# Kernel tuning notes

Measured on AMD Instinct MI355X. Metric: run time of the kernel, lower is better.

The kernel has to match this reference:

```python
import jax, jax.numpy as jnp
import numpy as np

B, S, D = 16, 1024, 64
BASE, SCALE = 10000.0, 1.0


def setup_inputs() -> dict:
    key = jax.random.key(0)
    # geospatial coordinates in [0, 1)
    spa_feat = jax.random.uniform(key, (B, S, 2), dtype=jnp.float32)
    return {"spa_feat": spa_feat}


def reference(spa_feat):
    d = D
    q = d // 4  # number of frequency bands per coordinate axis
    inv_freq = 1.0 / (BASE ** (jnp.arange(q, dtype=jnp.float32) / q))  # [q]
    xy = spa_feat * SCALE                                # [B,S,2]
    freq = xy[..., :, None] * inv_freq                   # [B,S,2,q]
    freq_x, freq_y = freq[..., 0, :], freq[..., 1, :]    # [B,S,q] each
    sin_emb = jnp.concatenate([jnp.sin(freq_x), jnp.sin(freq_y)], axis=-1)  # [B,S,d/2]
    cos_emb = jnp.concatenate([jnp.cos(freq_x), jnp.cos(freq_y)], axis=-1)  # [B,S,d/2]
    b, s, h = sin_emb.shape  # h = d//2 number of 2x2 blocks
    r = 2 * jnp.arange(h)    # top-left row/col index of each 2x2 block
    # Block-diagonal rotation matrix: block i = [[cos_i, -sin_i], [sin_i, cos_i]]
    R = jnp.zeros((b, s, d, d), dtype=sin_emb.dtype)
    R = (R.at[:, :, r, r].set(cos_emb)
           .at[:, :, r, r + 1].set(-sin_emb)
           .at[:, :, r + 1, r].set(sin_emb)
           .at[:, :, r + 1, r + 1].set(cos_emb))
    return R
```

## Files before the change

### kernel.cpp

```cpp
#include <hip/hip_runtime.h>


#define NBS 16384
#define MPB 8
#define NBLK (NBS / MPB)

typedef float vfloat4 __attribute__((ext_vector_type(4)));

__global__ __launch_bounds__(256) void rope2d_kernel(
    const float* __restrict__ spa,
    float* __restrict__ out)
{
    const int t   = threadIdx.x;
    const int bs0 = blockIdx.x * MPB;

    __shared__ float ssin[MPB * 32];
    __shared__ float scos[MPB * 32];

    {
        const int m = t >> 5;
        const int h = t & 31;
        const float xy   = spa[(bs0 + m) * 2 + (h >> 4)];
        const int   i    = h & 15;
        const float invf = exp2f(-(float)i * 0.83048202372184059f);
        float s, c;
        sincosf(xy * invf, &s, &c);
        ssin[t] = s;
        scos[t] = c;
    }
    __syncthreads();

    vfloat4* outv = (vfloat4*)out + (size_t)bs0 * 1024;
    const int cg = t & 15;

    #pragma unroll
    for (int k = 0; k < 32; ++k) {
        const int g   = t + k * 256;
        const int row = (g >> 4) & 63;
        vfloat4 v = (vfloat4)(0.f, 0.f, 0.f, 0.f);
        if ((row >> 2) == cg) {
            const int m = g >> 10;
            const int h = row >> 1;
            const float s = ssin[m * 32 + h];
            const float c = scos[m * 32 + h];
            const float e0 = (row & 1) ? s : c;
            const float e1 = (row & 1) ? c : -s;
            if (row & 2) { v.z = e0; v.w = e1; }
            else         { v.x = e0; v.y = e1; }
        }
        __builtin_nontemporal_store(v, &outv[g]);
    }
}

extern "C" void kernel_launch(void* const* d_in, const int* in_sizes, int n_in,
                              void* d_out, int out_size, void* d_ws, size_t ws_size,
                              hipStream_t stream) {
    const float* spa = (const float*)d_in[0];
    float* out = (float*)d_out;
    rope2d_kernel<<<NBLK, 256, 0, stream>>>(spa, out);
}
```

Baseline: 265.0 us.

## Zero output with memset and scatter only diagonal-block vectors

Fills the whole output with hipMemsetAsync, then launches a kernel that writes only the four float4 chunks per row around the 2x2 diagonal block instead of all sixteen. The aim is to move most of the zero-filling into the driver's fill path and cut the work each thread does. In exchange, the output is written twice (a full memset plus a partial scatter), which adds total memory traffic. It also adds a second launch and drops the nontemporal store hint.

```diff
diff --git a/kernel.cpp b/kernel.cpp
--- a/kernel.cpp
+++ b/kernel.cpp
@@ -7,7 +7,7 @@
 
 typedef float vfloat4 __attribute__((ext_vector_type(4)));
 
-__global__ __launch_bounds__(256) void rope2d_kernel(
+__global__ __launch_bounds__(256) void rope2d_scatter_kernel(
     const float* __restrict__ spa,
     float* __restrict__ out)
 {
@@ -31,24 +31,23 @@
     __syncthreads();
 
     vfloat4* outv = (vfloat4*)out + (size_t)bs0 * 1024;
-    const int cg = t & 15;
 
     #pragma unroll
-    for (int k = 0; k < 32; ++k) {
-        const int g   = t + k * 256;
-        const int row = (g >> 4) & 63;
+    for (int j = 0; j < MPB; ++j) {
+        const int idx = t + j * 256;
+        const int m   = idx >> 8;
+        const int r   = (idx >> 2) & 63;
+        const int lj  = idx & 3;
         vfloat4 v = (vfloat4)(0.f, 0.f, 0.f, 0.f);
-        if ((row >> 2) == cg) {
-            const int m = g >> 10;
-            const int h = row >> 1;
-            const float s = ssin[m * 32 + h];
-            const float c = scos[m * 32 + h];
-            const float e0 = (row & 1) ? s : c;
-            const float e1 = (row & 1) ? c : -s;
-            if (row & 2) { v.z = e0; v.w = e1; }
-            else         { v.x = e0; v.y = e1; }
+        if (lj == ((r >> 2) & 3)) {
+            const float s = ssin[m * 32 + (r >> 1)];
+            const float c = scos[m * 32 + (r >> 1)];
+            const float e0 = (r & 1) ? s : c;
+            const float e1 = (r & 1) ? c : -s;
+            if (r & 2) { v.z = e0; v.w = e1; }
+            else       { v.x = e0; v.y = e1; }
         }
-        __builtin_nontemporal_store(v, &outv[g]);
+        outv[m * 1024 + r * 16 + (r >> 4) * 4 + lj] = v;
     }
 }
 
@@ -57,5 +56,6 @@
                               hipStream_t stream) {
     const float* spa = (const float*)d_in[0];
     float* out = (float*)d_out;
-    rope2d_kernel<<<NBLK, 256, 0, stream>>>(spa, out);
+    hipMemsetAsync(out, 0, (size_t)out_size * sizeof(float), stream);
+    rope2d_scatter_kernel<<<NBLK, 256, 0, stream>>>(spa, out);
 }
```

Result: faster. 259.4 us (-2.1%).
